# Kernel optimization log

Hardware: AMD Instinct MI355X
Metric: run time of the kernel (lower is better)

Reference implementation:

```python
import jax, jax.numpy as jnp
import numpy as np
import math

B, S, D, H, FF, L, V = 4, 2048, 512, 8, 2048, 4, 256
WINDOW, STRIDE, NGLOBAL = 256, 128, 16  # sparse pattern: causal & (local | strided | global)


def setup_inputs() -> dict:
    key = jax.random.key(0)
    ks = jax.random.split(key, 12)
    g = lambda k, shp: jax.random.normal(k, shp, dtype=jnp.float32) * 0.02
    return {
        "src_tokens": jax.random.randint(ks[0], (B, S), 0, V, dtype=jnp.int32),
        "emb": g(ks[1], (V, D)),
        "b_out": jnp.zeros((V,), jnp.float32),
        "Wq": g(ks[2], (L, D, D)), "bq": jnp.zeros((L, D), jnp.float32),
        "Wk": g(ks[3], (L, D, D)), "bk": jnp.zeros((L, D), jnp.float32),
        "Wv": g(ks[4], (L, D, D)), "bv": jnp.zeros((L, D), jnp.float32),
        "Wo": g(ks[5], (L, D, D)), "bo": jnp.zeros((L, D), jnp.float32),
        "ln1_g": jnp.ones((L, D), jnp.float32), "ln1_b": jnp.zeros((L, D), jnp.float32),
        "W1": g(ks[6], (L, D, FF)), "b1": jnp.zeros((L, FF), jnp.float32),
        "W2": g(ks[7], (L, FF, D)), "b2": jnp.zeros((L, D), jnp.float32),
        "ln2_g": jnp.ones((L, D), jnp.float32), "ln2_b": jnp.zeros((L, D), jnp.float32),
    }


def _pos_enc(seq_len, d_model):
    pos = jnp.arange(seq_len, dtype=jnp.float32)[:, None]
    div = jnp.exp(jnp.arange(0, d_model, 2, dtype=jnp.float32) * (-math.log(10000.0) / d_model))
    pe = jnp.zeros((seq_len, d_model), jnp.float32)
    pe = pe.at[:, 0::2].set(jnp.sin(pos * div)).at[:, 1::2].set(jnp.cos(pos * div))
    return pe


def _ln(x, g, b):
    m = x.mean(-1, keepdims=True)
    v = ((x - m) ** 2).mean(-1, keepdims=True)
    return (x - m) * jax.lax.rsqrt(v + 1e-5) * g + b


def _sparse_mask(seq_len):
    i = jnp.arange(seq_len)[:, None]
    j = jnp.arange(seq_len)[None, :]
    causal = j <= i
    local = (i - j) < WINDOW
    strided = ((i - j) % STRIDE) == 0
    glob = j < NGLOBAL
    return causal & (local | strided | glob)  # [S, S] bool


def reference(src_tokens, emb, b_out, Wq, bq, Wk, bk, Wv, bv, Wo, bo,
              ln1_g, ln1_b, W1, b1, W2, b2, ln2_g, ln2_b):
    dh = D // H
    x = emb[src_tokens] * math.sqrt(D) + _pos_enc(S, D)  # [B,S,D] (dropout inactive at eval)
    mask = _sparse_mask(S)
    for l in range(L):
        q = (x @ Wq[l] + bq[l]).reshape(B, S, H, dh)
        k = (x @ Wk[l] + bk[l]).reshape(B, S, H, dh)
        v = (x @ Wv[l] + bv[l]).reshape(B, S, H, dh)
        scores = jnp.einsum('bihd,bjhd->bhij', q, k) / math.sqrt(dh)
        scores = jnp.where(mask, scores, jnp.float32(-1e9))
        attn = jax.nn.softmax(scores, axis=-1)
        o = jnp.einsum('bhij,bjhd->bihd', attn, v).reshape(B, S, D)
        x = _ln(x + o @ Wo[l] + bo[l], ln1_g[l], ln1_b[l])      # post-LN residual
        h = jax.nn.relu(x @ W1[l] + b1[l])
        x = _ln(x + h @ W2[l] + b2[l], ln2_g[l], ln2_b[l])
    return x @ emb.T + b_out  # tied output projection -> [B,S,V]
```

## Files before the change

### kernel.cpp

```cpp
#include <hip/hip_runtime.h>
#include <hip/hip_bf16.h>
#include <math.h>

#define B_  4
#define S_  2048
#define D_  512
#define H_  8
#define DH_ 64
#define FF_ 2048
#define L_  4
#define V_  256
#define NTOK (B_ * S_)
#define XN  ((size_t)NTOK * D_)

typedef __attribute__((ext_vector_type(8))) short bf16x8;
typedef __attribute__((ext_vector_type(4))) float f32x4;
typedef __attribute__((ext_vector_type(8))) unsigned short u16x8;
typedef __attribute__((ext_vector_type(4))) unsigned short u16x4;

typedef const __attribute__((address_space(1))) unsigned int* gptr_u32;
typedef __attribute__((address_space(3))) unsigned int* lptr_u32;

__device__ __forceinline__ float bf2f(unsigned short u) {
    return __uint_as_float((unsigned)u << 16);
}
__device__ __forceinline__ unsigned short f2bf_bits(float f) {
    __hip_bfloat16 t = __float2bfloat16(f);
    return *(unsigned short*)&t;
}

__global__ void pe_table_kernel(float* __restrict__ PE) {
    int s = blockIdx.x;
    int d = threadIdx.x * 2;
    float ang = (float)s * expf((float)d * (-logf(10000.0f) / (float)D_));
    PE[(size_t)s * D_ + d]     = sinf(ang);
    PE[(size_t)s * D_ + d + 1] = cosf(ang);
}

__global__ void embed_kernel(const int* __restrict__ tok,
                             const float* __restrict__ emb,
                             const float* __restrict__ PE,
                             float* __restrict__ X,
                             __hip_bfloat16* __restrict__ Xb) {
    int bs = blockIdx.x;
    int s = bs % S_;
    int t = tok[bs];
    const float scale = 22.62741699796952f;
    int d = threadIdx.x * 4;
    float4 e = *(const float4*)(emb + (size_t)t * D_ + d);
    float4 p = *(const float4*)(PE + (size_t)s * D_ + d);
    float4 v = make_float4(e.x * scale + p.x, e.y * scale + p.y,
                           e.z * scale + p.z, e.w * scale + p.w);
    *(float4*)(X + (size_t)bs * D_ + d) = v;
    u16x4 pk = { f2bf_bits(v.x), f2bf_bits(v.y), f2bf_bits(v.z), f2bf_bits(v.w) };
    *(u16x4*)((unsigned short*)Xb + (size_t)bs * D_ + d) = pk;
}

__global__ void transpose_conv_kernel(const float* __restrict__ W,
                                      __hip_bfloat16* __restrict__ Wt,
                                      int K, int N) {
    const float* Wl = W + (size_t)blockIdx.z * K * N;
    __hip_bfloat16* Wtl = Wt + (size_t)blockIdx.z * K * N;
    __shared__ float t[32][33];
    int k0 = blockIdx.y * 32, n0 = blockIdx.x * 32;
    int tx = threadIdx.x & 31, ty = threadIdx.x >> 5;
    #pragma unroll
    for (int q = 0; q < 4; ++q)
        t[ty + q * 8][tx] = Wl[(size_t)(k0 + ty + q * 8) * N + n0 + tx];
    __syncthreads();
    #pragma unroll
    for (int q = 0; q < 4; ++q)
        Wtl[(size_t)(n0 + ty + q * 8) * K + k0 + tx] =
            __float2bfloat16(t[tx][ty + q * 8]);
}

__global__ void transpose_qkv_kernel(const float* __restrict__ Wq,
                                     const float* __restrict__ Wk,
                                     const float* __restrict__ Wv,
                                     __hip_bfloat16* __restrict__ dst) {
    int z = blockIdx.z, l = z / 3, which = z % 3;
    const float* src = (which == 0 ? Wq : which == 1 ? Wk : Wv) + (size_t)l * D_ * D_;
    __hip_bfloat16* d = dst + (size_t)l * 1536 * D_ + (size_t)which * D_ * D_;
    __shared__ float t[32][33];
    int k0 = blockIdx.y * 32, n0 = blockIdx.x * 32;
    int tx = threadIdx.x & 31, ty = threadIdx.x >> 5;
    #pragma unroll
    for (int q = 0; q < 4; ++q)
        t[ty + q * 8][tx] = src[(size_t)(k0 + ty + q * 8) * D_ + n0 + tx];
    __syncthreads();
    #pragma unroll
    for (int q = 0; q < 4; ++q)
        d[(size_t)(n0 + ty + q * 8) * D_ + k0 + tx] =
            __float2bfloat16(t[tx][ty + q * 8]);
}

__global__ void conv_bf16_kernel(const float* __restrict__ in,
                                 __hip_bfloat16* __restrict__ out, int n) {
    int i = blockIdx.x * 256 + threadIdx.x;
    if (i < n) out[i] = __float2bfloat16(in[i]);
}

template <int RELU, int OUT_MODE>
__global__ __launch_bounds__(256)
void gemm_bf16_kernel(const __hip_bfloat16* __restrict__ A,
                      const __hip_bfloat16* __restrict__ Bt,
                      const float* __restrict__ bias0,
                      const float* __restrict__ bias1,
                      const float* __restrict__ bias2,
                      float* __restrict__ Cf,
                      __hip_bfloat16* __restrict__ Cb0,
                      __hip_bfloat16* __restrict__ Cb1,
                      __hip_bfloat16* __restrict__ Cb2,
                      __hip_bfloat16* __restrict__ CbT,
                      int M, int N, int K) {
    __shared__ unsigned short As[2][128 * 32];
    __shared__ unsigned short Bs[2][128 * 32];
    int tid = threadIdx.x;
    int lane = tid & 63, wid = tid >> 6;
    int wm = (wid >> 1) * 64, wn = (wid & 1) * 64;
    int g = lane >> 4, il = lane & 15;

    int gx = gridDim.x;
    int fid = blockIdx.x + gx * blockIdx.y;
    int cpx = (gx * gridDim.y) >> 3;
    int swz = (fid & 7) * cpx + (fid >> 3);
    int m0 = (swz / gx) * 128, n0 = (swz % gx) * 128;

    auto stage = [&](int buf, int k0) {
        #pragma unroll
        for (int q = 0; q < 2; ++q) {
            int idx = q * 256 + tid;
            int r = idx >> 2, c = idx & 3;
            int csw = (c ^ r) & 3;
            const __hip_bfloat16* sa = A + (size_t)(m0 + r) * K + k0 + csw * 8;
            __builtin_amdgcn_global_load_lds((gptr_u32)(const void*)sa,
                                             (lptr_u32)(void*)&As[buf][idx * 8], 16, 0, 0);
            const __hip_bfloat16* sb = Bt + (size_t)(n0 + r) * K + k0 + csw * 8;
            __builtin_amdgcn_global_load_lds((gptr_u32)(const void*)sb,
                                             (lptr_u32)(void*)&Bs[buf][idx * 8], 16, 0, 0);
        }
    };

    f32x4 acc[4][4] = {};
    int NT = K >> 5;
    stage(0, 0);

    for (int t = 0; t < NT; ++t) {
        int cur = t & 1;
        if (t + 1 < NT) {
            stage(cur ^ 1, (t + 1) << 5);
            asm volatile("s_waitcnt vmcnt(4)" ::: "memory");
        } else {
            asm volatile("s_waitcnt vmcnt(0)" ::: "memory");
        }
        __builtin_amdgcn_s_barrier();

        bf16x8 af[4], bf[4];
        #pragma unroll
        for (int i = 0; i < 4; ++i) {
            int m = wm + i * 16 + il;
            af[i] = *(const bf16x8*)&As[cur][m * 32 + ((g ^ m) & 3) * 8];
            int n = wn + i * 16 + il;
            bf[i] = *(const bf16x8*)&Bs[cur][n * 32 + ((g ^ n) & 3) * 8];
        }
        #pragma unroll
        for (int i = 0; i < 4; ++i)
            #pragma unroll
            for (int j = 0; j < 4; ++j)
                acc[i][j] = __builtin_amdgcn_mfma_f32_16x16x32_bf16(
                    af[i], bf[j], acc[i][j], 0, 0, 0);

        __builtin_amdgcn_s_barrier();
    }

    if (OUT_MODE == 4) {
        int seg = n0 >> 9;
        const float* bias = seg == 0 ? bias0 : seg == 1 ? bias1 : bias2;
        __hip_bfloat16* Crow = seg == 0 ? Cb0 : seg == 1 ? Cb1 : Cb2;
        int nseg = n0 & 511;
        #pragma unroll
        for (int j = 0; j < 4; ++j) {
            int coll = nseg + wn + j * 16 + il;
            float bv = bias[coll];
            #pragma unroll
            for (int i = 0; i < 4; ++i) {
                int row0 = m0 + wm + i * 16 + g * 4;
                if (seg < 2) {
                    #pragma unroll
                    for (int r = 0; r < 4; ++r)
                        Crow[(size_t)(row0 + r) * 512 + coll] =
                            __float2bfloat16(acc[i][j][r] + bv);
                } else {
                    u16x4 pk;
                    #pragma unroll
                    for (int r = 0; r < 4; ++r) {
                        float v = acc[i][j][r] + bv;
                        Crow[(size_t)(row0 + r) * 512 + coll] = __float2bfloat16(v);
                        pk[r] = f2bf_bits(v);
                    }
                    int hh = coll >> 6, dh = coll & 63;
                    int bb = row0 >> 11, s0 = row0 & 2047;
                    *(u16x4*)(CbT + ((size_t)((bb * 8 + hh) * 64 + dh) * 2048 + s0)) = pk;
                }
            }
        }
    } else {
        #pragma unroll
        for (int j = 0; j < 4; ++j) {
            int col = n0 + wn + j * 16 + il;
            float bv = bias0[col];
            #pragma unroll
            for (int i = 0; i < 4; ++i) {
                #pragma unroll
                for (int r = 0; r < 4; ++r) {
                    int row = m0 + wm + i * 16 + g * 4 + r;
                    float v = acc[i][j][r] + bv;
                    if (RELU) v = fmaxf(v, 0.0f);
                    if (OUT_MODE == 1) Cb0[(size_t)row * N + col] = __float2bfloat16(v);
                    else               Cf[(size_t)row * N + col] = v;
                }
            }
        }
    }
}

__device__ __forceinline__ bf16x8 lds_frag(const unsigned short* base, int row, int chunk) {
    int byte = (row << 7) + (((chunk ^ (row & 7)) & 7) << 4);
    return *(const bf16x8*)((const char*)base + byte);
}

__global__ __launch_bounds__(256)
void attn_mfma_kernel(const __hip_bfloat16* __restrict__ Q,
                      const __hip_bfloat16* __restrict__ K,
                      const __hip_bfloat16* __restrict__ V,
                      const __hip_bfloat16* __restrict__ VT,
                      __hip_bfloat16* __restrict__ O) {
    __shared__ unsigned short Ks[2][64 * 64];
    __shared__ unsigned short Vs[2][64 * 64];
    __shared__ unsigned short Ps[4][16 * 64];

    int fid = blockIdx.x + 32 * (blockIdx.y + 8 * blockIdx.z);
    int swz = (fid & 7) * 128 + (fid >> 3);
    int i0 = (swz & 31) * 64;
    int h  = (swz >> 5) & 7;
    int b  = swz >> 8;

    int tid = threadIdx.x, lane = tid & 63, wv = tid >> 6;
    int g = lane >> 4, il = lane & 15, g4 = g * 4;

    int nloc = min(i0 >> 6, 4) + 1;
    int add0 = (i0 > 256);
    int nt = nloc + add0;

    const size_t vt_off = (size_t)((b * 8 + h) * 64) * 2048;
    auto j0_of = [&](int t) { return (t < nloc) ? (i0 - 64 * t) : 0; };

    auto stage = [&](int buf, int j0) {
        #pragma unroll
        for (int q = 0; q < 2; ++q) {
            int idx = q * 256 + tid;
            int row = idx >> 3, c = idx & 7;
            int csw = c ^ (row & 7);
            const __hip_bfloat16* sk = K + (size_t)(b * 2048 + j0 + row) * 512 + h * 64 + csw * 8;
            __builtin_amdgcn_global_load_lds((gptr_u32)(const void*)sk,
                                             (lptr_u32)(void*)&Ks[buf][idx * 8], 16, 0, 0);
            const __hip_bfloat16* sv = VT + vt_off + (size_t)row * 2048 + j0 + csw * 8;
            __builtin_amdgcn_global_load_lds((gptr_u32)(const void*)sv,
                                             (lptr_u32)(void*)&Vs[buf][idx * 8], 16, 0, 0);
        }
    };

    int iq = i0 + wv * 16 + il;
    bf16x8 qf[2];
    #pragma unroll
    for (int kh = 0; kh < 2; ++kh)
        qf[kh] = *(const bf16x8*)(Q + (size_t)(b * 2048 + iq) * 512 + h * 64 + kh * 32 + g * 8);

    stage(0, j0_of(0));

    float qfl[16];
    #pragma unroll
    for (int kh = 0; kh < 2; ++kh)
        #pragma unroll
        for (int e = 0; e < 8; ++e)
            qfl[kh * 8 + e] = bf2f(((u16x8)qf[kh])[e]);

    unsigned short* myP = Ps[wv];
    f32x4 o[4] = {};
    float os[16] = {};
    float m = -1e30f, l = 0.0f;
    const float CSC = 0.18033688011112042f;

    const unsigned short* Kbase = (const unsigned short*)(K + (size_t)b * 2048 * 512 + h * 64);
    const unsigned short* Vbase = (const unsigned short*)(V + (size_t)b * 2048 * 512 + h * 64);
    for (int j = iq - 384; j >= 16; j -= 128) {
        const unsigned short* kr = Kbase + (size_t)j * 512;
        u16x8 k0 = *(const u16x8*)(kr + g * 8);
        u16x8 k1 = *(const u16x8*)(kr + 32 + g * 8);
        float dot = 0.0f;
        #pragma unroll
        for (int e = 0; e < 8; ++e)
            dot += qfl[e] * bf2f(k0[e]) + qfl[8 + e] * bf2f(k1[e]);
        dot += __shfl_xor(dot, 16);
        dot += __shfl_xor(dot, 32);
        float s2 = dot * CSC;
        float mn = fmaxf(m, s2);
        float al = exp2f(m - mn);
        float p = exp2f(s2 - mn);
        l = l * al + p;
        m = mn;
        const unsigned short* vr = Vbase + (size_t)j * 512;
        u16x8 v0 = *(const u16x8*)(vr + g * 8);
        u16x8 v1 = *(const u16x8*)(vr + 32 + g * 8);
        #pragma unroll
        for (int e = 0; e < 8; ++e) {
            os[e]     = os[e]     * al + p * bf2f(v0[e]);
            os[8 + e] = os[8 + e] * al + p * bf2f(v1[e]);
        }
    }

    for (int t = 0; t < nt; ++t) {
        __syncthreads();
        int cur = t & 1;
        if (t + 1 < nt) stage(cur ^ 1, j0_of(t + 1));
        int j0 = j0_of(t);

        f32x4 s[4] = {};
        #pragma unroll
        for (int kh = 0; kh < 2; ++kh)
            #pragma unroll
            for (int jn = 0; jn < 4; ++jn) {
                bf16x8 a = lds_frag(Ks[cur], jn * 16 + il, kh * 4 + g);
                s[jn] = __builtin_amdgcn_mfma_f32_16x16x32_bf16(a, qf[kh], s[jn], 0, 0, 0);
            }

        float mloc = -1e30f;
        if (t >= nloc) {
            #pragma unroll
            for (int jn = 0; jn < 4; ++jn)
                #pragma unroll
                for (int r = 0; r < 4; ++r) {
                    int jg = jn * 16 + g4 + r;
                    float sv = (jg < 16) ? s[jn][r] * CSC : -1e30f;
                    s[jn][r] = sv;
                    mloc = fmaxf(mloc, sv);
                }
        } else if (t == 0) {
            #pragma unroll
            for (int jn = 0; jn < 4; ++jn)
                #pragma unroll
                for (int r = 0; r < 4; ++r) {
                    int jg = j0 + jn * 16 + g4 + r;
                    float sv = (iq >= jg) ? s[jn][r] * CSC : -1e30f;
                    s[jn][r] = sv;
                    mloc = fmaxf(mloc, sv);
                }
        } else if (t == 4) {
            #pragma unroll
            for (int jn = 0; jn < 4; ++jn)
                #pragma unroll
                for (int r = 0; r < 4; ++r) {
                    int jg = j0 + jn * 16 + g4 + r;
                    int dij = iq - jg;
                    bool ok = (dij < 256) || ((dij & 127) == 0) || (jg < 16);
                    float sv = ok ? s[jn][r] * CSC : -1e30f;
                    s[jn][r] = sv;
                    mloc = fmaxf(mloc, sv);
                }
        } else {
            #pragma unroll
            for (int jn = 0; jn < 4; ++jn)
                #pragma unroll
                for (int r = 0; r < 4; ++r) {
                    float sv = s[jn][r] * CSC;
                    s[jn][r] = sv;
                    mloc = fmaxf(mloc, sv);
                }
        }
        mloc = fmaxf(mloc, __shfl_xor(mloc, 16));
        mloc = fmaxf(mloc, __shfl_xor(mloc, 32));
        float mn = fmaxf(m, mloc);
        float al = exp2f(m - mn);

        float lloc = 0.0f;
        #pragma unroll
        for (int jn = 0; jn < 4; ++jn)
            #pragma unroll
            for (int r = 0; r < 4; ++r) {
                float p = exp2f(s[jn][r] - mn);
                s[jn][r] = p;
                lloc += p;
            }
        lloc += __shfl_xor(lloc, 16);
        lloc += __shfl_xor(lloc, 32);
        l = l * al + lloc;
        m = mn;

        if (!__all(al == 1.0f)) {
            float ar[4];
            #pragma unroll
            for (int r = 0; r < 4; ++r) ar[r] = __shfl(al, g4 + r);
            #pragma unroll
            for (int dn = 0; dn < 4; ++dn)
                #pragma unroll
                for (int r = 0; r < 4; ++r) o[dn][r] *= ar[r];
            #pragma unroll
            for (int e = 0; e < 16; ++e) os[e] *= al;
        }

        #pragma unroll
        for (int jn = 0; jn < 4; ++jn) {
            u16x4 pk;
            #pragma unroll
            for (int r = 0; r < 4; ++r) pk[r] = f2bf_bits(s[jn][r]);
            int byte = ((il << 7) + (jn << 5) + (g << 3)) ^ ((il & 7) << 4);
            *(u16x4*)((char*)myP + byte) = pk;
        }
        #pragma unroll
        for (int kh = 0; kh < 2; ++kh) {
            bf16x8 pa = lds_frag(myP, il, kh * 4 + g);
            #pragma unroll
            for (int dn = 0; dn < 4; ++dn) {
                bf16x8 bv = lds_frag(Vs[cur], dn * 16 + il, kh * 4 + g);
                o[dn] = __builtin_amdgcn_mfma_f32_16x16x32_bf16(pa, bv, o[dn], 0, 0, 0);
            }
        }
    }

    __syncthreads();
    float* osl = (float*)&Ks[0][0] + wv * 1024;
    #pragma unroll
    for (int kh = 0; kh < 2; ++kh)
        #pragma unroll
        for (int e = 0; e < 8; ++e)
            osl[il * 64 + kh * 32 + g * 8 + e] = os[kh * 8 + e];
    __syncthreads();

    float li[4];
    #pragma unroll
    for (int r = 0; r < 4; ++r) li[r] = 1.0f / __shfl(l, g4 + r);
    #pragma unroll
    for (int dn = 0; dn < 4; ++dn)
        #pragma unroll
        for (int r = 0; r < 4; ++r) {
            int row = i0 + wv * 16 + g4 + r;
            float add = osl[(g4 + r) * 64 + dn * 16 + il];
            O[(size_t)(b * 2048 + row) * 512 + h * 64 + dn * 16 + il] =
                __float2bfloat16((o[dn][r] + add) * li[r]);
        }
}

__global__ __launch_bounds__(256)
void add_ln_kernel(float* __restrict__ X,
                   const __hip_bfloat16* __restrict__ T,
                   const float* __restrict__ g,
                   const float* __restrict__ bb,
                   __hip_bfloat16* __restrict__ Xb) {
    size_t row = blockIdx.x * 4 + (threadIdx.x >> 6);
    int lane = threadIdx.x & 63;
    int d0 = lane * 8;
    float4 x0 = *(const float4*)(X + row * D_ + d0);
    float4 x1 = *(const float4*)(X + row * D_ + d0 + 4);
    u16x8 tv = *(const u16x8*)((const unsigned short*)T + row * D_ + d0);
    float v[8] = { x0.x + bf2f(tv[0]), x0.y + bf2f(tv[1]),
                   x0.z + bf2f(tv[2]), x0.w + bf2f(tv[3]),
                   x1.x + bf2f(tv[4]), x1.y + bf2f(tv[5]),
                   x1.z + bf2f(tv[6]), x1.w + bf2f(tv[7]) };
    float sum = 0.0f;
    #pragma unroll
    for (int q = 0; q < 8; ++q) sum += v[q];
    #pragma unroll
    for (int o = 32; o; o >>= 1) sum += __shfl_xor(sum, o);
    float mean = sum * (1.0f / D_);
    float var = 0.0f;
    #pragma unroll
    for (int q = 0; q < 8; ++q) { float dd = v[q] - mean; var += dd * dd; }
    #pragma unroll
    for (int o = 32; o; o >>= 1) var += __shfl_xor(var, o);
    var *= (1.0f / D_);
    float r = rsqrtf(var + 1e-5f);
    float4 g0 = *(const float4*)(g + d0),  g1 = *(const float4*)(g + d0 + 4);
    float4 b0 = *(const float4*)(bb + d0), b1 = *(const float4*)(bb + d0 + 4);
    float y[8];
    y[0] = (v[0]-mean)*r*g0.x+b0.x; y[1] = (v[1]-mean)*r*g0.y+b0.y;
    y[2] = (v[2]-mean)*r*g0.z+b0.z; y[3] = (v[3]-mean)*r*g0.w+b0.w;
    y[4] = (v[4]-mean)*r*g1.x+b1.x; y[5] = (v[5]-mean)*r*g1.y+b1.y;
    y[6] = (v[6]-mean)*r*g1.z+b1.z; y[7] = (v[7]-mean)*r*g1.w+b1.w;
    *(float4*)(X + row * D_ + d0)     = make_float4(y[0], y[1], y[2], y[3]);
    *(float4*)(X + row * D_ + d0 + 4) = make_float4(y[4], y[5], y[6], y[7]);
    u16x8 pk;
    #pragma unroll
    for (int q = 0; q < 8; ++q) pk[q] = f2bf_bits(y[q]);
    *(u16x8*)((unsigned short*)Xb + row * D_ + d0) = pk;
}

extern "C" void kernel_launch(void* const* d_in, const int* in_sizes, int n_in,
                              void* d_out, int out_size, void* d_ws, size_t ws_size,
                              hipStream_t stream) {
    const int*   tok   = (const int*)  d_in[0];
    const float* emb   = (const float*)d_in[1];
    const float* b_out = (const float*)d_in[2];
    const float* Wq    = (const float*)d_in[3];
    const float* bq    = (const float*)d_in[4];
    const float* Wk    = (const float*)d_in[5];
    const float* bk    = (const float*)d_in[6];
    const float* Wv    = (const float*)d_in[7];
    const float* bv    = (const float*)d_in[8];
    const float* Wo    = (const float*)d_in[9];
    const float* bo    = (const float*)d_in[10];
    const float* ln1g  = (const float*)d_in[11];
    const float* ln1b  = (const float*)d_in[12];
    const float* W1    = (const float*)d_in[13];
    const float* b1    = (const float*)d_in[14];
    const float* W2    = (const float*)d_in[15];
    const float* b2    = (const float*)d_in[16];
    const float* ln2g  = (const float*)d_in[17];
    const float* ln2b  = (const float*)d_in[18];
    float* out = (float*)d_out;

    char* w = (char*)d_ws;
    auto alloc = [&](size_t bytes) {
        char* p = w;
        w += (bytes + 255) & ~(size_t)255;
        return p;
    };
    float*          X   = (float*)         alloc(XN * 4);
    __hip_bfloat16* Xb  = (__hip_bfloat16*)alloc(XN * 2);
    __hip_bfloat16* Tb  = (__hip_bfloat16*)alloc(XN * 2);
    char* uni = alloc(XN * 2 * 5);
    __hip_bfloat16* Qb  = (__hip_bfloat16*)uni;
    __hip_bfloat16* Kb  = Qb + XN;
    __hip_bfloat16* Vb  = Kb + XN;
    __hip_bfloat16* VTb = Vb + XN;
    __hip_bfloat16* Ob  = VTb + XN;
    __hip_bfloat16* Hb  = (__hip_bfloat16*)uni;
    __hip_bfloat16* Wqkvt = (__hip_bfloat16*)alloc((size_t)L_ * 1536 * D_ * 2);
    __hip_bfloat16* Wot  = (__hip_bfloat16*)alloc((size_t)L_ * D_ * D_ * 2);
    __hip_bfloat16* W1t  = (__hip_bfloat16*)alloc((size_t)L_ * D_ * FF_ * 2);
    __hip_bfloat16* W2t  = (__hip_bfloat16*)alloc((size_t)L_ * FF_ * D_ * 2);
    __hip_bfloat16* embb = (__hip_bfloat16*)alloc((size_t)V_ * D_ * 2);
    float*          PE   = (float*)alloc((size_t)S_ * D_ * 4);

    {
        pe_table_kernel<<<S_, 256, 0, stream>>>(PE);
        dim3 gqkv(D_ / 32, D_ / 32, L_ * 3);
        transpose_qkv_kernel<<<gqkv, 256, 0, stream>>>(Wq, Wk, Wv, Wqkvt);
        dim3 gdd(D_ / 32, D_ / 32, L_);
        transpose_conv_kernel<<<gdd, 256, 0, stream>>>(Wo, Wot, D_, D_);
        dim3 g1(FF_ / 32, D_ / 32, L_);
        transpose_conv_kernel<<<g1, 256, 0, stream>>>(W1, W1t, D_, FF_);
        dim3 g2(D_ / 32, FF_ / 32, L_);
        transpose_conv_kernel<<<g2, 256, 0, stream>>>(W2, W2t, FF_, D_);
        conv_bf16_kernel<<<(V_ * D_ + 255) / 256, 256, 0, stream>>>(emb, embb, V_ * D_);
    }

    embed_kernel<<<NTOK, 128, 0, stream>>>(tok, emb, PE, X, Xb);

    dim3 blk(256);
    dim3 gqkv(1536 / 128, NTOK / 128);
    dim3 g512(D_ / 128, NTOK / 128);
    dim3 gff (FF_ / 128, NTOK / 128);
    dim3 gout(V_ / 128, NTOK / 128);
    dim3 gattn(S_ / 64, H_, B_);
    dim3 gln(NTOK / 4);

    for (int l = 0; l < L_; ++l) {
        const __hip_bfloat16* wqkv = Wqkvt + (size_t)l * 1536 * D_;
        const __hip_bfloat16* wot = Wot + (size_t)l * D_ * D_;
        const __hip_bfloat16* w1t = W1t + (size_t)l * D_ * FF_;
        const __hip_bfloat16* w2t = W2t + (size_t)l * FF_ * D_;

        gemm_bf16_kernel<0, 4><<<gqkv, blk, 0, stream>>>(
            Xb, wqkv, bq + l * D_, bk + l * D_, bv + l * D_,
            nullptr, Qb, Kb, Vb, VTb, NTOK, 1536, D_);

        attn_mfma_kernel<<<gattn, blk, 0, stream>>>(Qb, Kb, Vb, VTb, Ob);

        gemm_bf16_kernel<0, 1><<<g512, blk, 0, stream>>>(
            Ob, wot, bo + l * D_, nullptr, nullptr,
            nullptr, Tb, nullptr, nullptr, nullptr, NTOK, D_, D_);
        add_ln_kernel<<<gln, blk, 0, stream>>>(X, Tb, ln1g + l * D_, ln1b + l * D_, Xb);

        gemm_bf16_kernel<1, 1><<<gff, blk, 0, stream>>>(
            Xb, w1t, b1 + l * FF_, nullptr, nullptr,
            nullptr, Hb, nullptr, nullptr, nullptr, NTOK, FF_, D_);
        gemm_bf16_kernel<0, 1><<<g512, blk, 0, stream>>>(
            Hb, w2t, b2 + l * D_, nullptr, nullptr,
            nullptr, Tb, nullptr, nullptr, nullptr, NTOK, D_, FF_);
        add_ln_kernel<<<gln, blk, 0, stream>>>(X, Tb, ln2g + l * D_, ln2b + l * D_, Xb);
    }

    gemm_bf16_kernel<0, 0><<<gout, blk, 0, stream>>>(
        Xb, embb, b_out, nullptr, nullptr,
        out, nullptr, nullptr, nullptr, nullptr, NTOK, V_, D_);
}
```

Baseline: 711.1 us.

## Add BM=64 GEMM tile for narrow outputs and skip masked attention MFMAs

The GEMM kernel takes the M-tile height as a template parameter, and the N=512 and vocab projections use 64-row tiles. This doubles their grid size so more workgroups fill the CUs. The attention kernel skips QK and PV MFMAs for global-token tiles (only the first 16 keys are valid) and for the upper-triangular parts of the diagonal tile. It also raises wave priority around the MFMA sections. Smaller tiles reread the B operand more often, and the branchy per-tile paths may add divergence or register pressure.

```diff
diff --git a/kernel.cpp b/kernel.cpp
--- a/kernel.cpp
+++ b/kernel.cpp
@@ -100,7 +100,7 @@
     if (i < n) out[i] = __float2bfloat16(in[i]);
 }
 
-template <int RELU, int OUT_MODE>
+template <int BM, int RELU, int OUT_MODE>
 __global__ __launch_bounds__(256)
 void gemm_bf16_kernel(const __hip_bfloat16* __restrict__ A,
                       const __hip_bfloat16* __restrict__ Bt,
@@ -113,35 +113,42 @@
                       __hip_bfloat16* __restrict__ Cb2,
                       __hip_bfloat16* __restrict__ CbT,
                       int M, int N, int K) {
-    __shared__ unsigned short As[2][128 * 32];
+    constexpr int MI = BM / 32;
+    __shared__ unsigned short As[2][BM * 32];
     __shared__ unsigned short Bs[2][128 * 32];
     int tid = threadIdx.x;
     int lane = tid & 63, wid = tid >> 6;
-    int wm = (wid >> 1) * 64, wn = (wid & 1) * 64;
+    int wm = (wid >> 1) * (BM / 2), wn = (wid & 1) * 64;
     int g = lane >> 4, il = lane & 15;
 
     int gx = gridDim.x;
     int fid = blockIdx.x + gx * blockIdx.y;
     int cpx = (gx * gridDim.y) >> 3;
     int swz = (fid & 7) * cpx + (fid >> 3);
-    int m0 = (swz / gx) * 128, n0 = (swz % gx) * 128;
+    int m0 = (swz / gx) * BM, n0 = (swz % gx) * 128;
 
     auto stage = [&](int buf, int k0) {
         #pragma unroll
-        for (int q = 0; q < 2; ++q) {
+        for (int q = 0; q < BM / 64; ++q) {
             int idx = q * 256 + tid;
             int r = idx >> 2, c = idx & 3;
             int csw = (c ^ r) & 3;
             const __hip_bfloat16* sa = A + (size_t)(m0 + r) * K + k0 + csw * 8;
             __builtin_amdgcn_global_load_lds((gptr_u32)(const void*)sa,
                                              (lptr_u32)(void*)&As[buf][idx * 8], 16, 0, 0);
+        }
+        #pragma unroll
+        for (int q = 0; q < 2; ++q) {
+            int idx = q * 256 + tid;
+            int r = idx >> 2, c = idx & 3;
+            int csw = (c ^ r) & 3;
             const __hip_bfloat16* sb = Bt + (size_t)(n0 + r) * K + k0 + csw * 8;
             __builtin_amdgcn_global_load_lds((gptr_u32)(const void*)sb,
                                              (lptr_u32)(void*)&Bs[buf][idx * 8], 16, 0, 0);
         }
     };
 
-    f32x4 acc[4][4] = {};
+    f32x4 acc[MI][4] = {};
     int NT = K >> 5;
     stage(0, 0);
 
@@ -149,22 +156,28 @@
         int cur = t & 1;
         if (t + 1 < NT) {
             stage(cur ^ 1, (t + 1) << 5);
-            asm volatile("s_waitcnt vmcnt(4)" ::: "memory");
+            if constexpr (BM == 128)
+                asm volatile("s_waitcnt vmcnt(4)" ::: "memory");
+            else
+                asm volatile("s_waitcnt vmcnt(3)" ::: "memory");
         } else {
             asm volatile("s_waitcnt vmcnt(0)" ::: "memory");
         }
         __builtin_amdgcn_s_barrier();
 
-        bf16x8 af[4], bf[4];
-        #pragma unroll
-        for (int i = 0; i < 4; ++i) {
+        bf16x8 af[MI], bf[4];
+        #pragma unroll
+        for (int i = 0; i < MI; ++i) {
             int m = wm + i * 16 + il;
             af[i] = *(const bf16x8*)&As[cur][m * 32 + ((g ^ m) & 3) * 8];
-            int n = wn + i * 16 + il;
-            bf[i] = *(const bf16x8*)&Bs[cur][n * 32 + ((g ^ n) & 3) * 8];
-        }
-        #pragma unroll
-        for (int i = 0; i < 4; ++i)
+        }
+        #pragma unroll
+        for (int j = 0; j < 4; ++j) {
+            int n = wn + j * 16 + il;
+            bf[j] = *(const bf16x8*)&Bs[cur][n * 32 + ((g ^ n) & 3) * 8];
+        }
+        #pragma unroll
+        for (int i = 0; i < MI; ++i)
             #pragma unroll
             for (int j = 0; j < 4; ++j)
                 acc[i][j] = __builtin_amdgcn_mfma_f32_16x16x32_bf16(
@@ -173,7 +186,7 @@
         __builtin_amdgcn_s_barrier();
     }
 
-    if (OUT_MODE == 4) {
+    if constexpr (OUT_MODE == 4) {
         int seg = n0 >> 9;
         const float* bias = seg == 0 ? bias0 : seg == 1 ? bias1 : bias2;
         __hip_bfloat16* Crow = seg == 0 ? Cb0 : seg == 1 ? Cb1 : Cb2;
@@ -183,7 +196,7 @@
             int coll = nseg + wn + j * 16 + il;
             float bv = bias[coll];
             #pragma unroll
-            for (int i = 0; i < 4; ++i) {
+            for (int i = 0; i < MI; ++i) {
                 int row0 = m0 + wm + i * 16 + g * 4;
                 if (seg < 2) {
                     #pragma unroll
@@ -210,7 +223,7 @@
             int col = n0 + wn + j * 16 + il;
             float bv = bias0[col];
             #pragma unroll
-            for (int i = 0; i < 4; ++i) {
+            for (int i = 0; i < MI; ++i) {
                 #pragma unroll
                 for (int r = 0; r < 4; ++r) {
                     int row = m0 + wm + i * 16 + g * 4 + r;
@@ -324,37 +337,64 @@
         int cur = t & 1;
         if (t + 1 < nt) stage(cur ^ 1, j0_of(t + 1));
         int j0 = j0_of(t);
+        bool gtile = (t >= nloc);
+        bool dtile = (t == 0);
 
         f32x4 s[4] = {};
-        #pragma unroll
-        for (int kh = 0; kh < 2; ++kh)
+        __builtin_amdgcn_s_setprio(1);
+        if (gtile) {
+            #pragma unroll
+            for (int kh = 0; kh < 2; ++kh) {
+                bf16x8 a = lds_frag(Ks[cur], il, kh * 4 + g);
+                s[0] = __builtin_amdgcn_mfma_f32_16x16x32_bf16(a, qf[kh], s[0], 0, 0, 0);
+            }
+        } else if (dtile) {
+            #pragma unroll
+            for (int kh = 0; kh < 2; ++kh)
+                #pragma unroll
+                for (int jn = 0; jn < 4; ++jn)
+                    if (jn <= wv) {
+                        bf16x8 a = lds_frag(Ks[cur], jn * 16 + il, kh * 4 + g);
+                        s[jn] = __builtin_amdgcn_mfma_f32_16x16x32_bf16(a, qf[kh], s[jn], 0, 0, 0);
+                    }
+        } else {
+            #pragma unroll
+            for (int kh = 0; kh < 2; ++kh)
+                #pragma unroll
+                for (int jn = 0; jn < 4; ++jn) {
+                    bf16x8 a = lds_frag(Ks[cur], jn * 16 + il, kh * 4 + g);
+                    s[jn] = __builtin_amdgcn_mfma_f32_16x16x32_bf16(a, qf[kh], s[jn], 0, 0, 0);
+                }
+        }
+        __builtin_amdgcn_s_setprio(0);
+
+        float mloc = -1e30f;
+        if (gtile) {
+            #pragma unroll
+            for (int r = 0; r < 4; ++r) {
+                float sv = s[0][r] * CSC;
+                s[0][r] = sv;
+                mloc = fmaxf(mloc, sv);
+            }
+        } else if (dtile) {
             #pragma unroll
             for (int jn = 0; jn < 4; ++jn) {
-                bf16x8 a = lds_frag(Ks[cur], jn * 16 + il, kh * 4 + g);
-                s[jn] = __builtin_amdgcn_mfma_f32_16x16x32_bf16(a, qf[kh], s[jn], 0, 0, 0);
-            }
-
-        float mloc = -1e30f;
-        if (t >= nloc) {
-            #pragma unroll
-            for (int jn = 0; jn < 4; ++jn)
-                #pragma unroll
-                for (int r = 0; r < 4; ++r) {
-                    int jg = jn * 16 + g4 + r;
-                    float sv = (jg < 16) ? s[jn][r] * CSC : -1e30f;
-                    s[jn][r] = sv;
-                    mloc = fmaxf(mloc, sv);
-                }
-        } else if (t == 0) {
-            #pragma unroll
-            for (int jn = 0; jn < 4; ++jn)
-                #pragma unroll
-                for (int r = 0; r < 4; ++r) {
-                    int jg = j0 + jn * 16 + g4 + r;
-                    float sv = (iq >= jg) ? s[jn][r] * CSC : -1e30f;
-                    s[jn][r] = sv;
-                    mloc = fmaxf(mloc, sv);
-                }
+                if (jn < wv) {
+                    #pragma unroll
+                    for (int r = 0; r < 4; ++r) {
+                        float sv = s[jn][r] * CSC;
+                        s[jn][r] = sv;
+                        mloc = fmaxf(mloc, sv);
+                    }
+                } else if (jn == wv) {
+                    #pragma unroll
+                    for (int r = 0; r < 4; ++r) {
+                        float sv = (g4 + r <= il) ? s[jn][r] * CSC : -1e30f;
+                        s[jn][r] = sv;
+                        mloc = fmaxf(mloc, sv);
+                    }
+                }
+            }
         } else if (t == 4) {
             #pragma unroll
             for (int jn = 0; jn < 4; ++jn)
@@ -383,14 +423,25 @@
         float al = exp2f(m - mn);
 
         float lloc = 0.0f;
-        #pragma unroll
-        for (int jn = 0; jn < 4; ++jn)
+        if (gtile) {
             #pragma unroll
             for (int r = 0; r < 4; ++r) {
-                float p = exp2f(s[jn][r] - mn);
-                s[jn][r] = p;
+                float p = exp2f(s[0][r] - mn);
+                s[0][r] = p;
                 lloc += p;
             }
+        } else {
+            #pragma unroll
+            for (int jn = 0; jn < 4; ++jn) {
+                if (dtile && jn > wv) continue;
+                #pragma unroll
+                for (int r = 0; r < 4; ++r) {
+                    float p = exp2f(s[jn][r] - mn);
+                    s[jn][r] = p;
+                    lloc += p;
+                }
+            }
+        }
         lloc += __shfl_xor(lloc, 16);
         lloc += __shfl_xor(lloc, 32);
         l = l * al + lloc;
@@ -410,21 +461,30 @@
 
         #pragma unroll
         for (int jn = 0; jn < 4; ++jn) {
-            u16x4 pk;
-            #pragma unroll
-            for (int r = 0; r < 4; ++r) pk[r] = f2bf_bits(s[jn][r]);
+            if (gtile && jn >= 2) continue;
+            u16x4 pk = { 0, 0, 0, 0 };
+            bool live = gtile ? (jn == 0) : (!dtile || jn <= wv);
+            if (live) {
+                #pragma unroll
+                for (int r = 0; r < 4; ++r) pk[r] = f2bf_bits(s[jn][r]);
+            }
             int byte = ((il << 7) + (jn << 5) + (g << 3)) ^ ((il & 7) << 4);
             *(u16x4*)((char*)myP + byte) = pk;
         }
+        int khmax = (gtile || (dtile && wv < 2)) ? 1 : 2;
+        __builtin_amdgcn_s_setprio(1);
         #pragma unroll
         for (int kh = 0; kh < 2; ++kh) {
-            bf16x8 pa = lds_frag(myP, il, kh * 4 + g);
-            #pragma unroll
-            for (int dn = 0; dn < 4; ++dn) {
-                bf16x8 bv = lds_frag(Vs[cur], dn * 16 + il, kh * 4 + g);
-                o[dn] = __builtin_amdgcn_mfma_f32_16x16x32_bf16(pa, bv, o[dn], 0, 0, 0);
-            }
-        }
+            if (kh < khmax) {
+                bf16x8 pa = lds_frag(myP, il, kh * 4 + g);
+                #pragma unroll
+                for (int dn = 0; dn < 4; ++dn) {
+                    bf16x8 bv = lds_frag(Vs[cur], dn * 16 + il, kh * 4 + g);
+                    o[dn] = __builtin_amdgcn_mfma_f32_16x16x32_bf16(pa, bv, o[dn], 0, 0, 0);
+                }
+            }
+        }
+        __builtin_amdgcn_s_setprio(0);
     }
 
     __syncthreads();
@@ -558,9 +618,9 @@
 
     dim3 blk(256);
     dim3 gqkv(1536 / 128, NTOK / 128);
-    dim3 g512(D_ / 128, NTOK / 128);
+    dim3 g512n(D_ / 128, NTOK / 64);
     dim3 gff (FF_ / 128, NTOK / 128);
-    dim3 gout(V_ / 128, NTOK / 128);
+    dim3 gout(V_ / 128, NTOK / 64);
     dim3 gattn(S_ / 64, H_, B_);
     dim3 gln(NTOK / 4);
 
@@ -570,27 +630,27 @@
         const __hip_bfloat16* w1t = W1t + (size_t)l * D_ * FF_;
         const __hip_bfloat16* w2t = W2t + (size_t)l * FF_ * D_;
 
-        gemm_bf16_kernel<0, 4><<<gqkv, blk, 0, stream>>>(
+        gemm_bf16_kernel<128, 0, 4><<<gqkv, blk, 0, stream>>>(
             Xb, wqkv, bq + l * D_, bk + l * D_, bv + l * D_,
             nullptr, Qb, Kb, Vb, VTb, NTOK, 1536, D_);
 
         attn_mfma_kernel<<<gattn, blk, 0, stream>>>(Qb, Kb, Vb, VTb, Ob);
 
-        gemm_bf16_kernel<0, 1><<<g512, blk, 0, stream>>>(
+        gemm_bf16_kernel<64, 0, 1><<<g512n, blk, 0, stream>>>(
             Ob, wot, bo + l * D_, nullptr, nullptr,
             nullptr, Tb, nullptr, nullptr, nullptr, NTOK, D_, D_);
         add_ln_kernel<<<gln, blk, 0, stream>>>(X, Tb, ln1g + l * D_, ln1b + l * D_, Xb);
 
-        gemm_bf16_kernel<1, 1><<<gff, blk, 0, stream>>>(
+        gemm_bf16_kernel<128, 1, 1><<<gff, blk, 0, stream>>>(
             Xb, w1t, b1 + l * FF_, nullptr, nullptr,
             nullptr, Hb, nullptr, nullptr, nullptr, NTOK, FF_, D_);
-        gemm_bf16_kernel<0, 1><<<g512, blk, 0, stream>>>(
+        gemm_bf16_kernel<64, 0, 1><<<g512n, blk, 0, stream>>>(
             Hb, w2t, b2 + l * D_, nullptr, nullptr,
             nullptr, Tb, nullptr, nullptr, nullptr, NTOK, D_, FF_);
         add_ln_kernel<<<gln, blk, 0, stream>>>(X, Tb, ln2g + l * D_, ln2b + l * D_, Xb);
     }
 
-    gemm_bf16_kernel<0, 0><<<gout, blk, 0, stream>>>(
+    gemm_bf16_kernel<64, 0, 0><<<gout, blk, 0, stream>>>(
         Xb, embb, b_out, nullptr, nullptr,
         out, nullptr, nullptr, nullptr, nullptr, NTOK, V_, D_);
 }
```

Measured after the change: 692.5 us. -2.6%, faster.
